# Kernel tuning notes

Hardware: AMD Instinct MI355X
Metric: run time of the kernel (lower is better)

The kernel has to match this reference:

```python
import jax, jax.numpy as jnp
import numpy as np

N, D, P = 8192, 512, 3
TEMP, SIM_TH, DIS_TH, CLIP = 0.1, 0.15, 0.35, 30.0
NEG = -1e9  # finite stand-in for -inf mask (exp underflows to 0 identically)


def setup_inputs() -> dict:
    key = jax.random.key(0)
    k1, k2 = jax.random.split(key)
    embeddings = jax.random.normal(k1, (N, D), dtype=jnp.float32)
    thetas = jax.random.uniform(k2, (N, P), dtype=jnp.float32)
    return {"embeddings": embeddings, "thetas": thetas}


def reference(embeddings, thetas):
    n = embeddings.shape[0]
    # F.normalize(dim=-1)
    e = embeddings / jnp.maximum(
        jnp.linalg.norm(embeddings, axis=-1, keepdims=True), 1e-12)
    sim = jnp.clip(e @ e.T / TEMP, -CLIP, CLIP)  # [N, N]

    # cdist(thetas, thetas) normalized by its max; only feeds boolean masks
    t = jax.lax.stop_gradient(thetas)
    sq = jnp.sum(t * t, axis=1)
    d2 = jnp.maximum(sq[:, None] + sq[None, :] - 2.0 * (t @ t.T), 0.0)
    dist = jnp.sqrt(d2)
    dist = dist / (dist.max() + 1e-8)

    eye = jnp.eye(n, dtype=bool)
    pos = (dist < SIM_TH) & ~eye      # positives (self excluded: diag is -inf masked)
    neg = dist > DIS_TH               # negatives (diag never included: dist==0)
    sel = pos | neg

    # per-row cross_entropy over logits [pos_idx; neg_idx] with label 0 is:
    #   -sim[i, first_pos_index(i)] + logsumexp_{j in sel(i)} sim[i, j]
    masked = jnp.where(sel, sim, NEG)
    denom = jax.nn.logsumexp(masked, axis=1)            # [N]
    tgt = jnp.argmax(pos, axis=1)                       # first positive index
    tgt_logit = jnp.take_along_axis(sim, tgt[:, None], axis=1)[:, 0]
    valid = pos.any(axis=1) & neg.any(axis=1)
    per_row = jnp.where(valid, denom - tgt_logit, 0.0)
    cnt = valid.sum()
    return jnp.where(cnt > 0, per_row.sum() / jnp.maximum(cnt, 1), 0.0)
```

## Files before the change

### kernel.cpp

```cpp
#include <hip/hip_runtime.h>

#define N 8192
#define D 512

typedef __attribute__((ext_vector_type(8))) short short8;
typedef __attribute__((ext_vector_type(4))) float f32x4;

typedef const __attribute__((address_space(1))) unsigned int* gas_t;
typedef __attribute__((address_space(3))) unsigned int* las_t;

static __device__ __forceinline__ unsigned short f2bf(float f) {
    unsigned u = __float_as_uint(f);
    unsigned r = (u + 0x7FFFu + ((u >> 16) & 1u)) >> 16;
    return (unsigned short)r;
}
static __device__ __forceinline__ float bf2f(unsigned u) {
    return __uint_as_float(u << 16);
}
static __device__ __forceinline__ void gl_lds16(const unsigned short* g, char* l) {
    __builtin_amdgcn_global_load_lds((gas_t)g, (las_t)l, 16, 0, 0);
}
static __device__ __forceinline__ int tri_cum(int r) { return r * (129 - r) / 2; }

__global__ void kpack(const float* __restrict__ th, float4* __restrict__ th4,
                      float* __restrict__ srow, unsigned* __restrict__ jminrow,
                      unsigned* __restrict__ negrow, unsigned* __restrict__ d2mb) {
    int i = blockIdx.x * 256 + threadIdx.x;
    if (i < N) {
        float x = th[3 * i], y = th[3 * i + 1], z = th[3 * i + 2];
        float4 v; v.x = x; v.y = y; v.z = z; v.w = x * x + y * y + z * z;
        th4[i] = v;
        srow[i] = 0.0f;
        jminrow[i] = 0xFFFFFFFFu;
        negrow[i] = 0u;
    }
    if (i == 0) *d2mb = 0u;
}

__global__ void knorm(const float* __restrict__ emb, unsigned short* __restrict__ e,
                      const float4* __restrict__ th4, unsigned* __restrict__ d2mb) {
    int w    = threadIdx.x >> 6;
    int row  = blockIdx.x * 4 + w;
    int lane = threadIdx.x & 63;
    const float4* src = (const float4*)(emb + (size_t)row * D);
    float4 v0 = src[lane * 2];
    float4 v1 = src[lane * 2 + 1];
    float ss = v0.x*v0.x + v0.y*v0.y + v0.z*v0.z + v0.w*v0.w
             + v1.x*v1.x + v1.y*v1.y + v1.z*v1.z + v1.w*v1.w;
#pragma unroll
    for (int off = 1; off < 64; off <<= 1) ss += __shfl_xor(ss, off, 64);
    float inv = 3.7982826f / fmaxf(sqrtf(ss), 1e-12f);
    unsigned short h0 = f2bf(v0.x * inv), h1 = f2bf(v0.y * inv);
    unsigned short h2 = f2bf(v0.z * inv), h3 = f2bf(v0.w * inv);
    unsigned short h4 = f2bf(v1.x * inv), h5 = f2bf(v1.y * inv);
    unsigned short h6 = f2bf(v1.z * inv), h7 = f2bf(v1.w * inv);
    uint4 pk;
    pk.x = (unsigned)h0 | ((unsigned)h1 << 16);
    pk.y = (unsigned)h2 | ((unsigned)h3 << 16);
    pk.z = (unsigned)h4 | ((unsigned)h5 << 16);
    pk.w = (unsigned)h6 | ((unsigned)h7 << 16);
    ((uint4*)(e + (size_t)row * D))[lane] = pk;

    if (blockIdx.x < 256) {
        int widx = blockIdx.x * 4 + w;
        int q0 = widx * 4;
        int m0 = N - 4 - q0;
        float4 a0 = th4[q0], a1 = th4[q0 + 1], a2 = th4[q0 + 2], a3 = th4[q0 + 3];
        float4 b0 = th4[m0], b1 = th4[m0 + 1], b2 = th4[m0 + 2], b3 = th4[m0 + 3];
        float m = 0.0f;
        for (int j = q0 + 1 + lane; j < N; j += 64) {
            float4 tj = th4[j];
            float d;
            d = a0.w + tj.w - 2.0f * (a0.x*tj.x + a0.y*tj.y + a0.z*tj.z); m = fmaxf(m, d);
            d = a1.w + tj.w - 2.0f * (a1.x*tj.x + a1.y*tj.y + a1.z*tj.z); m = fmaxf(m, d);
            d = a2.w + tj.w - 2.0f * (a2.x*tj.x + a2.y*tj.y + a2.z*tj.z); m = fmaxf(m, d);
            d = a3.w + tj.w - 2.0f * (a3.x*tj.x + a3.y*tj.y + a3.z*tj.z); m = fmaxf(m, d);
        }
        for (int j = m0 + 1 + lane; j < N; j += 64) {
            float4 tj = th4[j];
            float d;
            d = b0.w + tj.w - 2.0f * (b0.x*tj.x + b0.y*tj.y + b0.z*tj.z); m = fmaxf(m, d);
            d = b1.w + tj.w - 2.0f * (b1.x*tj.x + b1.y*tj.y + b1.z*tj.z); m = fmaxf(m, d);
            d = b2.w + tj.w - 2.0f * (b2.x*tj.x + b2.y*tj.y + b2.z*tj.z); m = fmaxf(m, d);
            d = b3.w + tj.w - 2.0f * (b3.x*tj.x + b3.y*tj.y + b3.z*tj.z); m = fmaxf(m, d);
        }
#pragma unroll
        for (int off = 1; off < 64; off <<= 1) m = fmaxf(m, __shfl_xor(m, off, 64));
        if (lane == 0) atomicMax(d2mb, __float_as_uint(m));
    }
}

__global__ __launch_bounds__(256) void kmain(
    const unsigned short* __restrict__ e, const float4* __restrict__ th4,
    const unsigned* __restrict__ d2mb, float* __restrict__ srow,
    unsigned* __restrict__ jminrow, unsigned* __restrict__ negrow) {
    __shared__ __align__(16) char smem[32768];

    const int tid  = threadIdx.x;
    const int lane = tid & 63;
    const int w    = tid >> 6;
    const int wr   = w >> 1;
    const int wc   = w & 1;

    const int bid = (int)blockIdx.x;
    const int swz = (bid & 7) * 260 + (bid >> 3);
    int rb = (int)((129.0f - sqrtf(16641.0f - 8.0f * (float)swz)) * 0.5f);
    rb = rb < 0 ? 0 : (rb > 63 ? 63 : rb);
    while (tri_cum(rb + 1) <= swz) rb++;
    while (tri_cum(rb) > swz) rb--;
    const int cb = rb + (swz - tri_cum(rb));
    const bool isdiag = (rb == cb);
    const int r0 = rb * 128, c0 = cb * 128;

    const int ssw = (((tid & 3) ^ ((tid >> 3) & 3)) << 3);
    const unsigned short* pA0 = e + (size_t)(r0 + (tid >> 2)) * D + ssw;
    const unsigned short* pA1 = pA0 + (size_t)64 * D;
    const unsigned short* pB0 = e + (size_t)(c0 + (tid >> 2)) * D + ssw;
    const unsigned short* pB1 = pB0 + (size_t)64 * D;

    const int fr = lane & 15;
    const int fq = lane >> 4;
    const int kslot = (fq ^ ((fr >> 1) & 3)) << 4;

    f32x4 acc[4][4];
#pragma unroll
    for (int mt = 0; mt < 4; mt++)
#pragma unroll
        for (int nt = 0; nt < 4; nt++) acc[mt][nt] = (f32x4){0.f, 0.f, 0.f, 0.f};

#define STAGE(T, BUF) { \
    const int k0_ = (T) * 32; char* d_ = smem + (BUF) * 16384;   \
    gl_lds16(pA0 + k0_, d_ + tid * 16);                          \
    gl_lds16(pA1 + k0_, d_ + 4096 + tid * 16);                   \
    gl_lds16(pB0 + k0_, d_ + 8192 + tid * 16);                   \
    gl_lds16(pB1 + k0_, d_ + 12288 + tid * 16); }

#define COMPUTE(BUF) { \
    const char* cA_ = smem + (BUF) * 16384;                      \
    const char* cB_ = cA_ + 8192;                                \
    short8 a_[4], b_[4];                                         \
    _Pragma("unroll")                                            \
    for (int mt = 0; mt < 4; mt++)                               \
        a_[mt] = *(const short8*)(cA_ + (wr * 64 + mt * 16 + fr) * 64 + kslot); \
    _Pragma("unroll")                                            \
    for (int nt = 0; nt < 4; nt++)                               \
        b_[nt] = *(const short8*)(cB_ + (wc * 64 + nt * 16 + fr) * 64 + kslot); \
    _Pragma("unroll")                                            \
    for (int mt = 0; mt < 4; mt++)                               \
    _Pragma("unroll")                                            \
    for (int nt = 0; nt < 4; nt++)                               \
        acc[mt][nt] = __builtin_amdgcn_mfma_f32_16x16x32_bf16(   \
            a_[mt], b_[nt], acc[mt][nt], 0, 0, 0); }

#define KST(T)                                                    \
    if ((T) + 1 < 16) STAGE((T) + 1, ((T) + 1) & 1)               \
    COMPUTE((T) & 1)                                              \
    asm volatile("s_waitcnt vmcnt(0)" ::: "memory");              \
    __builtin_amdgcn_s_barrier();                                 \
    __builtin_amdgcn_sched_barrier(0);

    STAGE(0, 0)
    asm volatile("s_waitcnt vmcnt(0)" ::: "memory");
    __builtin_amdgcn_s_barrier();
    __builtin_amdgcn_sched_barrier(0);
    KST(0)  KST(1)  KST(2)  KST(3)
    KST(4)  KST(5)  KST(6)  KST(7)
    KST(8)  KST(9)  KST(10) KST(11)
    KST(12) KST(13) KST(14) KST(15)
#undef KST
#undef COMPUTE
#undef STAGE
    __syncthreads();

    const float dmax = sqrtf(__uint_as_float(*d2mb)) + 1e-8f;
    const float p2 = 0.0225f * dmax * dmax;
    const float n2 = 0.1225f * dmax * dmax;

    const int j0 = c0 + wc * 64 + fr;
    float4 thj[4];
#pragma unroll
    for (int nt = 0; nt < 4; nt++) thj[nt] = th4[j0 + nt * 16];

    float*    lds_rs = (float*)smem;
    unsigned* lds_rj = (unsigned*)(smem + 1024);
    unsigned* lds_rn = (unsigned*)(smem + 2048);
    float*    lds_cs = (float*)(smem + 3072);
    unsigned* lds_cj = (unsigned*)(smem + 4096);
    unsigned* lds_cn = (unsigned*)(smem + 5120);

    float    csum[4]; unsigned cjm[4], cng[4];
#pragma unroll
    for (int nt = 0; nt < 4; nt++) { csum[nt] = 0.0f; cjm[nt] = 0xFFFFFFFFu; cng[nt] = 0u; }

    const int i0 = r0 + wr * 64 + fq * 4;
#pragma unroll
    for (int mt = 0; mt < 4; mt++) {
#pragma unroll
        for (int rr = 0; rr < 4; rr++) {
            const int i = i0 + mt * 16 + rr;
            const float4 ti = th4[i];
            float sv = 0.0f; unsigned jv = 0xFFFFFFFFu, nv = 0u;
#pragma unroll
            for (int nt = 0; nt < 4; nt++) {
                const int j = j0 + nt * 16;
                const float4 tj = thj[nt];
                float dot = ti.x * tj.x + ti.y * tj.y + ti.z * tj.z;
                float d2 = fmaf(-2.0f, dot, ti.w + tj.w);
                bool pos = isdiag ? ((d2 < p2) && (j != i)) : (d2 < p2);
                bool neg = (d2 > n2);
                float c = (pos || neg) ? exp2f(acc[mt][nt][rr]) : 0.0f;
                sv += c;
                if (neg) nv = 1u;
                if (pos) jv = min(jv, (unsigned)j);
                if (!isdiag) {
                    csum[nt] += c;
                    if (neg) cng[nt] = 1u;
                    if (pos) cjm[nt] = min(cjm[nt], (unsigned)i);
                }
            }
#pragma unroll
            for (int off = 1; off < 16; off <<= 1) {
                sv += __shfl_xor(sv, off, 64);
                jv = min(jv, (unsigned)__shfl_xor((int)jv, off, 64));
                nv |= (unsigned)__shfl_xor((int)nv, off, 64);
            }
            if (fr == 0) {
                const int rl = wr * 64 + mt * 16 + fq * 4 + rr;
                lds_rs[wc * 128 + rl] = sv;
                lds_rj[wc * 128 + rl] = jv;
                lds_rn[wc * 128 + rl] = nv;
            }
        }
    }

    if (!isdiag) {
#pragma unroll
        for (int nt = 0; nt < 4; nt++) {
            float sv = csum[nt]; unsigned jv = cjm[nt], nv = cng[nt];
#pragma unroll
            for (int off = 16; off < 64; off <<= 1) {
                sv += __shfl_xor(sv, off, 64);
                jv = min(jv, (unsigned)__shfl_xor((int)jv, off, 64));
                nv |= (unsigned)__shfl_xor((int)nv, off, 64);
            }
            if (fq == 0) {
                const int cl = wc * 64 + nt * 16 + fr;
                lds_cs[wr * 128 + cl] = sv;
                lds_cj[wr * 128 + cl] = jv;
                lds_cn[wr * 128 + cl] = nv;
            }
        }
    }
    __syncthreads();
    if (tid < 128) {
        float    sv = lds_rs[tid] + lds_rs[128 + tid];
        unsigned jv = min(lds_rj[tid], lds_rj[128 + tid]);
        unsigned nv = lds_rn[tid] | lds_rn[128 + tid];
        atomicAdd(&srow[r0 + tid], sv);
        atomicMin(&jminrow[r0 + tid], jv);
        atomicOr(&negrow[r0 + tid], nv);
        if (!isdiag) {
            float    cv = lds_cs[tid] + lds_cs[128 + tid];
            unsigned cj = min(lds_cj[tid], lds_cj[128 + tid]);
            unsigned cn = lds_cn[tid] | lds_cn[128 + tid];
            atomicAdd(&srow[c0 + tid], cv);
            atomicMin(&jminrow[c0 + tid], cj);
            atomicOr(&negrow[c0 + tid], cn);
        }
    }
}

__global__ void krow(const unsigned short* __restrict__ e, const float* __restrict__ srow,
                     const unsigned* __restrict__ jminrow, const unsigned* __restrict__ negrow,
                     float* __restrict__ pr, float* __restrict__ vf) {
    int row  = blockIdx.x * 4 + (threadIdx.x >> 6);
    int lane = threadIdx.x & 63;
    unsigned jmv = jminrow[row];
    bool valid = (jmv != 0xFFFFFFFFu) && (negrow[row] != 0u);
    float p = 0.0f;
    if (valid) {
        const uint4* a = (const uint4*)(e + (size_t)row * D);
        const uint4* b = (const uint4*)(e + (size_t)jmv * D);
        uint4 va = a[lane], vb = b[lane];
        float dot = 0.0f;
        dot += bf2f(va.x & 0xFFFFu) * bf2f(vb.x & 0xFFFFu);
        dot += bf2f(va.x >> 16)     * bf2f(vb.x >> 16);
        dot += bf2f(va.y & 0xFFFFu) * bf2f(vb.y & 0xFFFFu);
        dot += bf2f(va.y >> 16)     * bf2f(vb.y >> 16);
        dot += bf2f(va.z & 0xFFFFu) * bf2f(vb.z & 0xFFFFu);
        dot += bf2f(va.z >> 16)     * bf2f(vb.z >> 16);
        dot += bf2f(va.w & 0xFFFFu) * bf2f(vb.w & 0xFFFFu);
        dot += bf2f(va.w >> 16)     * bf2f(vb.w >> 16);
#pragma unroll
        for (int off = 1; off < 64; off <<= 1) dot += __shfl_xor(dot, off, 64);
        p = logf(srow[row]) - dot * 0.69314718f;
    }
    if (lane == 0) { pr[row] = p; vf[row] = valid ? 1.0f : 0.0f; }
}

__global__ void kfinal(const float* __restrict__ pr, const float* __restrict__ vf,
                       float* __restrict__ out) {
    __shared__ float ls[1024];
    __shared__ float lc[1024];
    int t = threadIdx.x;
    float sv = 0.0f, cv = 0.0f;
#pragma unroll
    for (int k = 0; k < 8; k++) { sv += pr[t * 8 + k]; cv += vf[t * 8 + k]; }
    ls[t] = sv; lc[t] = cv;
    __syncthreads();
    for (int off = 512; off > 0; off >>= 1) {
        if (t < off) { ls[t] += ls[t + off]; lc[t] += lc[t + off]; }
        __syncthreads();
    }
    if (t == 0) out[0] = (lc[0] > 0.0f) ? (ls[0] / lc[0]) : 0.0f;
}

extern "C" void kernel_launch(void* const* d_in, const int* in_sizes, int n_in,
                              void* d_out, int out_size, void* d_ws, size_t ws_size,
                              hipStream_t stream) {
    const float* emb = (const float*)d_in[0];
    const float* th  = (const float*)d_in[1];
    float* out = (float*)d_out;
    char* ws = (char*)d_ws;

    unsigned short* e    = (unsigned short*)(ws);
    float4*   th4        = (float4*)(ws + 8388608);
    float*    srow       = (float*)(ws + 8519680);
    unsigned* jminr      = (unsigned*)(ws + 8552448);
    unsigned* negr       = (unsigned*)(ws + 8585216);
    float*    pr         = (float*)(ws + 8617984);
    float*    vf         = (float*)(ws + 8650752);
    unsigned* d2mb       = (unsigned*)(ws + 8683520);

    kpack<<<32, 256, 0, stream>>>(th, th4, srow, jminr, negr, d2mb);
    knorm<<<N / 4, 256, 0, stream>>>(emb, e, th4, d2mb);
    kmain<<<2080, 256, 0, stream>>>(e, th4, d2mb, srow, jminr, negr);
    krow<<<N / 4, 256, 0, stream>>>(e, srow, jminr, negr, pr, vf);
    kfinal<<<1, 1024, 0, stream>>>(pr, vf, out);
}
```

Baseline: 127.0 us.

## Switch Gram matrix from bf16 to fp8 e4m3 MFMA

Normalized embeddings are quantized to fp8 (e4m3-style encoding done in software) instead of bf16, halving the bytes staged through LDS and the number of K stages. The main GEMM now uses the fp8 16x16x32 MFMA with two sub-steps per 64-wide K tile, and the row-target dot product in krow decodes the fp8 codes. The aim is higher matrix throughput and less memory traffic, at the cost of much lower precision in the similarity logits, which feed an exponential and could push the loss outside tolerance.

Measured after the change: 115.4 us. 1.1x faster.

```diff
diff --git a/kernel.cpp b/kernel.cpp
--- a/kernel.cpp
+++ b/kernel.cpp
@@ -3,24 +3,36 @@
 #define N 8192
 #define D 512
 
-typedef __attribute__((ext_vector_type(8))) short short8;
 typedef __attribute__((ext_vector_type(4))) float f32x4;
 
 typedef const __attribute__((address_space(1))) unsigned int* gas_t;
 typedef __attribute__((address_space(3))) unsigned int* las_t;
 
-static __device__ __forceinline__ unsigned short f2bf(float f) {
+static __device__ __forceinline__ void gl_lds16(const void* g, char* l) {
+    __builtin_amdgcn_global_load_lds((gas_t)g, (las_t)l, 16, 0, 0);
+}
+static __device__ __forceinline__ int tri_cum(int r) { return r * (129 - r) / 2; }
+
+static __device__ __forceinline__ unsigned f2fp8(float f) {
     unsigned u = __float_as_uint(f);
-    unsigned r = (u + 0x7FFFu + ((u >> 16) & 1u)) >> 16;
-    return (unsigned short)r;
-}
-static __device__ __forceinline__ float bf2f(unsigned u) {
-    return __uint_as_float(u << 16);
-}
-static __device__ __forceinline__ void gl_lds16(const unsigned short* g, char* l) {
-    __builtin_amdgcn_global_load_lds((gas_t)g, (las_t)l, 16, 0, 0);
-}
-static __device__ __forceinline__ int tri_cum(int r) { return r * (129 - r) / 2; }
+    unsigned sgn = (u >> 24) & 0x80u;
+    unsigned a = u & 0x7FFFFFFFu;
+    if (a >= 0x3C800000u) {
+        unsigned t = a + 0x7FFFFu + ((a >> 20) & 1u);
+        unsigned code = (((t >> 23) - 120u) << 3) | ((t >> 20) & 7u);
+        if (code > 0x7Eu) code = 0x7Eu;
+        return sgn | code;
+    }
+    float af = __uint_as_float(a);
+    unsigned m = (unsigned)(af * 512.0f + 0.5f);
+    return sgn | (m > 8u ? 8u : m);
+}
+static __device__ __forceinline__ float fp82f(unsigned c) {
+    unsigned e = (c >> 3) & 15u, m = c & 7u;
+    float v = (e == 0u) ? (float)m * 0.001953125f
+                        : __uint_as_float(((e + 120u) << 23) | (m << 20));
+    return (c & 0x80u) ? -v : v;
+}
 
 __global__ void kpack(const float* __restrict__ th, float4* __restrict__ th4,
                       float* __restrict__ srow, unsigned* __restrict__ jminrow,
@@ -37,7 +49,7 @@
     if (i == 0) *d2mb = 0u;
 }
 
-__global__ void knorm(const float* __restrict__ emb, unsigned short* __restrict__ e,
+__global__ void knorm(const float* __restrict__ emb, unsigned char* __restrict__ e,
                       const float4* __restrict__ th4, unsigned* __restrict__ d2mb) {
     int w    = threadIdx.x >> 6;
     int row  = blockIdx.x * 4 + w;
@@ -50,16 +62,14 @@
 #pragma unroll
     for (int off = 1; off < 64; off <<= 1) ss += __shfl_xor(ss, off, 64);
     float inv = 3.7982826f / fmaxf(sqrtf(ss), 1e-12f);
-    unsigned short h0 = f2bf(v0.x * inv), h1 = f2bf(v0.y * inv);
-    unsigned short h2 = f2bf(v0.z * inv), h3 = f2bf(v0.w * inv);
-    unsigned short h4 = f2bf(v1.x * inv), h5 = f2bf(v1.y * inv);
-    unsigned short h6 = f2bf(v1.z * inv), h7 = f2bf(v1.w * inv);
-    uint4 pk;
-    pk.x = (unsigned)h0 | ((unsigned)h1 << 16);
-    pk.y = (unsigned)h2 | ((unsigned)h3 << 16);
-    pk.z = (unsigned)h4 | ((unsigned)h5 << 16);
-    pk.w = (unsigned)h6 | ((unsigned)h7 << 16);
-    ((uint4*)(e + (size_t)row * D))[lane] = pk;
+    unsigned c0 = f2fp8(v0.x * inv), c1 = f2fp8(v0.y * inv);
+    unsigned c2 = f2fp8(v0.z * inv), c3 = f2fp8(v0.w * inv);
+    unsigned c4 = f2fp8(v1.x * inv), c5 = f2fp8(v1.y * inv);
+    unsigned c6 = f2fp8(v1.z * inv), c7 = f2fp8(v1.w * inv);
+    uint2 pk;
+    pk.x = c0 | (c1 << 8) | (c2 << 16) | (c3 << 24);
+    pk.y = c4 | (c5 << 8) | (c6 << 16) | (c7 << 24);
+    ((uint2*)(e + (size_t)row * D))[lane] = pk;
 
     if (blockIdx.x < 256) {
         int widx = blockIdx.x * 4 + w;
@@ -91,7 +101,7 @@
 }
 
 __global__ __launch_bounds__(256) void kmain(
-    const unsigned short* __restrict__ e, const float4* __restrict__ th4,
+    const unsigned char* __restrict__ e, const float4* __restrict__ th4,
     const unsigned* __restrict__ d2mb, float* __restrict__ srow,
     unsigned* __restrict__ jminrow, unsigned* __restrict__ negrow) {
     __shared__ __align__(16) char smem[32768];
@@ -112,15 +122,15 @@
     const bool isdiag = (rb == cb);
     const int r0 = rb * 128, c0 = cb * 128;
 
-    const int ssw = (((tid & 3) ^ ((tid >> 3) & 3)) << 3);
-    const unsigned short* pA0 = e + (size_t)(r0 + (tid >> 2)) * D + ssw;
-    const unsigned short* pA1 = pA0 + (size_t)64 * D;
-    const unsigned short* pB0 = e + (size_t)(c0 + (tid >> 2)) * D + ssw;
-    const unsigned short* pB1 = pB0 + (size_t)64 * D;
+    const int ssw = (((tid & 3) ^ ((tid >> 3) & 3)) << 4);
+    const unsigned char* pA0 = e + (size_t)(r0 + (tid >> 2)) * D + ssw;
+    const unsigned char* pA1 = pA0 + (size_t)64 * D;
+    const unsigned char* pB0 = e + (size_t)(c0 + (tid >> 2)) * D + ssw;
+    const unsigned char* pB1 = pB0 + (size_t)64 * D;
 
     const int fr = lane & 15;
     const int fq = lane >> 4;
-    const int kslot = (fq ^ ((fr >> 1) & 3)) << 4;
+    const int kslot0 = ((((fq >> 1) ^ ((fr >> 1) & 3)) << 4) | ((fq & 1) << 3));
 
     f32x4 acc[4][4];
 #pragma unroll
@@ -129,7 +139,7 @@
         for (int nt = 0; nt < 4; nt++) acc[mt][nt] = (f32x4){0.f, 0.f, 0.f, 0.f};
 
 #define STAGE(T, BUF) { \
-    const int k0_ = (T) * 32; char* d_ = smem + (BUF) * 16384;   \
+    const int k0_ = (T) * 64; char* d_ = smem + (BUF) * 16384;   \
     gl_lds16(pA0 + k0_, d_ + tid * 16);                          \
     gl_lds16(pA1 + k0_, d_ + 4096 + tid * 16);                   \
     gl_lds16(pB0 + k0_, d_ + 8192 + tid * 16);                   \
@@ -138,22 +148,26 @@
 #define COMPUTE(BUF) { \
     const char* cA_ = smem + (BUF) * 16384;                      \
     const char* cB_ = cA_ + 8192;                                \
-    short8 a_[4], b_[4];                                         \
     _Pragma("unroll")                                            \
-    for (int mt = 0; mt < 4; mt++)                               \
-        a_[mt] = *(const short8*)(cA_ + (wr * 64 + mt * 16 + fr) * 64 + kslot); \
-    _Pragma("unroll")                                            \
-    for (int nt = 0; nt < 4; nt++)                               \
-        b_[nt] = *(const short8*)(cB_ + (wc * 64 + nt * 16 + fr) * 64 + kslot); \
-    _Pragma("unroll")                                            \
-    for (int mt = 0; mt < 4; mt++)                               \
-    _Pragma("unroll")                                            \
-    for (int nt = 0; nt < 4; nt++)                               \
-        acc[mt][nt] = __builtin_amdgcn_mfma_f32_16x16x32_bf16(   \
-            a_[mt], b_[nt], acc[mt][nt], 0, 0, 0); }
+    for (int ks = 0; ks < 2; ++ks) {                             \
+        const int kb = kslot0 ^ (ks << 5);                       \
+        long a_[4], b_[4];                                       \
+        _Pragma("unroll")                                        \
+        for (int mt = 0; mt < 4; mt++)                           \
+            a_[mt] = *(const long*)(cA_ + (wr * 64 + mt * 16 + fr) * 64 + kb); \
+        _Pragma("unroll")                                        \
+        for (int nt = 0; nt < 4; nt++)                           \
+            b_[nt] = *(const long*)(cB_ + (wc * 64 + nt * 16 + fr) * 64 + kb); \
+        _Pragma("unroll")                                        \
+        for (int mt = 0; mt < 4; mt++)                           \
+        _Pragma("unroll")                                        \
+        for (int nt = 0; nt < 4; nt++)                           \
+            acc[mt][nt] = __builtin_amdgcn_mfma_f32_16x16x32_fp8_fp8( \
+                a_[mt], b_[nt], acc[mt][nt], 0, 0, 0);           \
+    } }
 
 #define KST(T)                                                    \
-    if ((T) + 1 < 16) STAGE((T) + 1, ((T) + 1) & 1)               \
+    if ((T) + 1 < 8) STAGE((T) + 1, ((T) + 1) & 1)                \
     COMPUTE((T) & 1)                                              \
     asm volatile("s_waitcnt vmcnt(0)" ::: "memory");              \
     __builtin_amdgcn_s_barrier();                                 \
@@ -165,8 +179,6 @@
     __builtin_amdgcn_sched_barrier(0);
     KST(0)  KST(1)  KST(2)  KST(3)
     KST(4)  KST(5)  KST(6)  KST(7)
-    KST(8)  KST(9)  KST(10) KST(11)
-    KST(12) KST(13) KST(14) KST(15)
 #undef KST
 #undef COMPUTE
 #undef STAGE
@@ -270,7 +282,7 @@
     }
 }
 
-__global__ void krow(const unsigned short* __restrict__ e, const float* __restrict__ srow,
+__global__ void krow(const unsigned char* __restrict__ e, const float* __restrict__ srow,
                      const unsigned* __restrict__ jminrow, const unsigned* __restrict__ negrow,
                      float* __restrict__ pr, float* __restrict__ vf) {
     int row  = blockIdx.x * 4 + (threadIdx.x >> 6);
@@ -279,18 +291,16 @@
     bool valid = (jmv != 0xFFFFFFFFu) && (negrow[row] != 0u);
     float p = 0.0f;
     if (valid) {
-        const uint4* a = (const uint4*)(e + (size_t)row * D);
-        const uint4* b = (const uint4*)(e + (size_t)jmv * D);
-        uint4 va = a[lane], vb = b[lane];
+        const uint2* a = (const uint2*)(e + (size_t)row * D);
+        const uint2* b = (const uint2*)(e + (size_t)jmv * D);
+        uint2 va = a[lane], vb = b[lane];
         float dot = 0.0f;
-        dot += bf2f(va.x & 0xFFFFu) * bf2f(vb.x & 0xFFFFu);
-        dot += bf2f(va.x >> 16)     * bf2f(vb.x >> 16);
-        dot += bf2f(va.y & 0xFFFFu) * bf2f(vb.y & 0xFFFFu);
-        dot += bf2f(va.y >> 16)     * bf2f(vb.y >> 16);
-        dot += bf2f(va.z & 0xFFFFu) * bf2f(vb.z & 0xFFFFu);
-        dot += bf2f(va.z >> 16)     * bf2f(vb.z >> 16);
-        dot += bf2f(va.w & 0xFFFFu) * bf2f(vb.w & 0xFFFFu);
-        dot += bf2f(va.w >> 16)     * bf2f(vb.w >> 16);
+#pragma unroll
+        for (int k = 0; k < 4; k++)
+            dot += fp82f((va.x >> (8 * k)) & 0xFFu) * fp82f((vb.x >> (8 * k)) & 0xFFu);
+#pragma unroll
+        for (int k = 0; k < 4; k++)
+            dot += fp82f((va.y >> (8 * k)) & 0xFFu) * fp82f((vb.y >> (8 * k)) & 0xFFu);
 #pragma unroll
         for (int off = 1; off < 64; off <<= 1) dot += __shfl_xor(dot, off, 64);
         p = logf(srow[row]) - dot * 0.69314718f;
@@ -323,7 +333,7 @@
     float* out = (float*)d_out;
     char* ws = (char*)d_ws;
 
-    unsigned short* e    = (unsigned short*)(ws);
+    unsigned char* e     = (unsigned char*)(ws);
     float4*   th4        = (float4*)(ws + 8388608);
     float*    srow       = (float*)(ws + 8519680);
     unsigned* jminr      = (unsigned*)(ws + 8552448);
```
